# Kernel tuning notes

Measured on AMD Instinct MI355X. Metric: run time of the kernel, lower is better.

## Reference

```python
import jax, jax.numpy as jnp
import numpy as np

D_MODEL = 1024
D_STATE = 16
D_CONV = 4
D_INNER = 2 * D_MODEL          # expand * d_model
DT_RANK = (D_MODEL + 15) // 16 # ceil(d_model/16) = 64
BATCH, SEQLEN = 2, 1024


def setup_inputs() -> dict:
    key = jax.random.key(0)
    ks = jax.random.split(key, 8)
    s = lambda k, shape, scale=0.02: (jax.random.normal(k, shape, jnp.float32) * scale)
    return {
        "hidden_states": jax.random.normal(ks[0], (BATCH, SEQLEN, D_MODEL), jnp.float32),
        "in_proj_w": s(ks[1], (2 * D_INNER, D_MODEL)),
        "conv_w": s(ks[2], (D_INNER, 1, D_CONV), 0.3),   # depthwise conv kernel (O, I/groups=1, K)
        "conv_b": jnp.zeros((D_INNER,), jnp.float32),
        "x_proj_w": s(ks[3], (DT_RANK + 2 * D_STATE, D_INNER)),
        "dt_proj_w": s(ks[4], (D_INNER, DT_RANK), 0.1),
        # inverse-softplus of small dt values, like the torch init
        "dt_proj_b": jax.random.uniform(ks[5], (D_INNER,), jnp.float32, minval=-5.0, maxval=-2.0),
        "A_log": jnp.log(jnp.broadcast_to(jnp.arange(1, D_STATE + 1, dtype=jnp.float32), (D_INNER, D_STATE))),
        "D": jnp.ones((D_INNER,), jnp.float32),
        "out_proj_w": s(ks[6], (D_MODEL, D_INNER)),
    }


def _forward(hidden_states, in_proj_w, conv_w, conv_b, x_proj_w,
             dt_proj_w, dt_proj_b, A_log, D, out_proj_w):
    B, L, _ = hidden_states.shape
    # in_proj -> split into x, z
    xz = hidden_states @ in_proj_w.T                      # [B, L, 2*d_inner]
    x, z = jnp.split(xz, 2, axis=-1)
    # causal depthwise conv1d (pad left d_conv-1, then take first L) + SiLU
    xc = jnp.transpose(x, (0, 2, 1))                      # [B, d_inner, L]
    xc = jax.lax.conv_general_dilated(
        xc, conv_w, window_strides=(1,), padding=[(D_CONV - 1, 0)],
        feature_group_count=D_INNER,
        dimension_numbers=("NCH", "OIH", "NCH")) + conv_b[None, :, None]
    xc = jax.nn.silu(xc)
    u = jnp.transpose(xc, (0, 2, 1)).astype(jnp.float32)  # [B, L, d_inner]
    # x_proj -> dt_low, B, C
    x_dbl = u @ x_proj_w.T                                # [B, L, dt_rank + 2*d_state]
    dt_low, Bp, Cp = jnp.split(x_dbl, [DT_RANK, DT_RANK + D_STATE], axis=-1)
    dt = dt_low @ dt_proj_w.T + dt_proj_b                 # [B, L, d_inner]
    # NOTE: original adds dt_proj.bias AGAIN as delta_bias inside the scan, then softplus
    delta = jax.nn.softplus(dt + dt_proj_b)
    A = -jnp.exp(A_log.astype(jnp.float32))               # [d_inner, d_state]
    # discretization
    dA = jnp.exp(jnp.einsum("bld,dn->lbdn", delta, A))    # [L, B, d, n]
    dBu = jnp.einsum("bld,bln,bld->lbdn", delta, Bp.astype(jnp.float32), u)
    C_t = jnp.transpose(Cp.astype(jnp.float32), (1, 0, 2))  # [L, B, n]

    def step(state, inp):
        a, b, c = inp
        state = a * state + b                             # [B, d, n]
        y = jnp.einsum("bdn,bn->bd", state, c)
        return state, y

    x0 = jnp.zeros((B, D_INNER, D_STATE), jnp.float32)
    _, ys = jax.lax.scan(step, x0, (dA, dBu, C_t))        # ys: [L, B, d]
    y = jnp.transpose(ys, (1, 0, 2))                      # [B, L, d]
    y = y + u * D.astype(jnp.float32)                     # skip connection
    y = y * jax.nn.silu(z.astype(jnp.float32))            # gating
    y = y.astype(hidden_states.dtype)
    return y @ out_proj_w.T                               # [B, L, d_model]


def reference(hidden_states, in_proj_w, conv_w, conv_b, x_proj_w,
              dt_proj_w, dt_proj_b, A_log, D, out_proj_w):
    return _forward(hidden_states, in_proj_w, conv_w, conv_b, x_proj_w,
                    dt_proj_w, dt_proj_b, A_log, D, out_proj_w)
```

## Files before the change

kernel.cpp:

```cpp
#include <hip/hip_runtime.h>
#include <hip/hip_bf16.h>
#include <math.h>

#define BATCH   2
#define SEQLEN  1024
#define DMODEL  1024
#define DINNER  2048
#define DSTATE  16
#define DTRANK  64
#define XPAD    128
#define MROWS   (BATCH*SEQLEN)
#define NSEG    8
#define SEGLEN  (SEQLEN/NSEG)
#define XP_SPLIT  8
#define OUT_SPLIT 2

typedef float    f32x4  __attribute__((ext_vector_type(4)));
typedef _Float16 f16x8  __attribute__((ext_vector_type(8)));
typedef _Float16 f16x4  __attribute__((ext_vector_type(4)));

template<int EPI>
__global__ __launch_bounds__(256) void pgemm64(
    const _Float16* __restrict__ A, int lda,
    const _Float16* __restrict__ W, int ldw,
    float* __restrict__ C, int ldc, int K,
    const float* __restrict__ bias, _Float16* __restrict__ C16, size_t zstride)
{
  constexpr int APS = 520;
  constexpr int BPS = 1032;
  __shared__ _Float16 As[2][8 * APS];
  __shared__ _Float16 Bs[2][8 * BPS];

  const int t  = threadIdx.x;
  const int m0 = blockIdx.y * 64, n0 = blockIdx.x * 128;
  const int kchunk = K / gridDim.z;
  const int kbeg = blockIdx.z * kchunk;
  const int nIter = kchunk / 64;

  const int kb = t & 7;
  const int r0 = t >> 3;
  const _Float16* gA = A + (size_t)(m0 + r0) * lda + kbeg + kb * 8;
  const _Float16* gB = W + (size_t)(n0 + r0) * ldw + kbeg + kb * 8;
  const size_t a32 = (size_t)32 * lda;
  const size_t b32 = (size_t)32 * ldw;
  const int aoff = kb * APS + r0 * 8;
  const int boff = kb * BPS + r0 * 8;

  {
    f16x8 a0 = *(const f16x8*)(gA);
    f16x8 a1 = *(const f16x8*)(gA + a32);
    f16x8 b0 = *(const f16x8*)(gB);
    f16x8 b1 = *(const f16x8*)(gB + b32);
    f16x8 b2 = *(const f16x8*)(gB + 2 * b32);
    f16x8 b3 = *(const f16x8*)(gB + 3 * b32);
    gA += 64; gB += 64;
    *(f16x8*)&As[0][aoff]       = a0;
    *(f16x8*)&As[0][aoff + 256] = a1;
    *(f16x8*)&Bs[0][boff]       = b0;
    *(f16x8*)&Bs[0][boff + 256] = b1;
    *(f16x8*)&Bs[0][boff + 512] = b2;
    *(f16x8*)&Bs[0][boff + 768] = b3;
  }

  const int lane = t & 63, wvi = t >> 6;
  const int wn = wvi * 32;
  const int lm = lane & 15, lk = lane >> 4;

  f32x4 acc[4][2] = {};

  for (int it = 0; it < nIter; ++it) {
    __syncthreads();
    const bool more = (it + 1 < nIter);
    f16x8 a0, a1, b0, b1, b2, b3;
    if (more) {
      a0 = *(const f16x8*)(gA);
      a1 = *(const f16x8*)(gA + a32);
      b0 = *(const f16x8*)(gB);
      b1 = *(const f16x8*)(gB + b32);
      b2 = *(const f16x8*)(gB + 2 * b32);
      b3 = *(const f16x8*)(gB + 3 * b32);
      gA += 64; gB += 64;
    }
    const int cb = it & 1;
#pragma unroll
    for (int s = 0; s < 2; ++s) {
      f16x8 av[4], bv[2];
#pragma unroll
      for (int i = 0; i < 4; ++i)
        av[i] = *(const f16x8*)&As[cb][(s * 4 + lk) * APS + (i * 16 + lm) * 8];
#pragma unroll
      for (int j = 0; j < 2; ++j)
        bv[j] = *(const f16x8*)&Bs[cb][(s * 4 + lk) * BPS + (wn + j * 16 + lm) * 8];
#pragma unroll
      for (int i = 0; i < 4; ++i)
#pragma unroll
        for (int j = 0; j < 2; ++j)
          acc[i][j] = __builtin_amdgcn_mfma_f32_16x16x32_f16(av[i], bv[j], acc[i][j], 0, 0, 0);
    }
    if (more) {
      const int nb = (it + 1) & 1;
      *(f16x8*)&As[nb][aoff]       = a0;
      *(f16x8*)&As[nb][aoff + 256] = a1;
      *(f16x8*)&Bs[nb][boff]       = b0;
      *(f16x8*)&Bs[nb][boff + 256] = b1;
      *(f16x8*)&Bs[nb][boff + 512] = b2;
      *(f16x8*)&Bs[nb][boff + 768] = b3;
    }
  }

  float* Cz = C + (size_t)blockIdx.z * zstride;
#pragma unroll
  for (int i = 0; i < 4; ++i) {
    const int mrow = m0 + i * 16 + lk * 4;
#pragma unroll
    for (int j = 0; j < 2; ++j) {
      const int col = n0 + wn + j * 16 + lm;
#pragma unroll
      for (int r = 0; r < 4; ++r) {
        float v = acc[i][j][r];
        size_t off = (size_t)(mrow + r) * ldc + col;
        if constexpr (EPI == 0) {
          Cz[off] = v;
        } else {
          float x = v + 2.f * bias[col];
          float sp = (x > 80.f) ? x : __logf(1.f + __expf(x));
          C16[off] = (_Float16)sp;
        }
      }
    }
  }
}

template<int EPI>
__global__ __launch_bounds__(256) void pgemm128(
    const _Float16* __restrict__ A, int lda,
    const _Float16* __restrict__ W, int ldw,
    float* __restrict__ C, int ldc, int K,
    _Float16* __restrict__ C16, size_t zstride)
{
  constexpr int PS = 1032;
  __shared__ _Float16 As[2][8 * PS];
  __shared__ _Float16 Bs[2][8 * PS];

  const int t  = threadIdx.x;
  const int m0 = blockIdx.y * 128, n0 = blockIdx.x * 128;
  const int kchunk = K / gridDim.z;
  const int kbeg = blockIdx.z * kchunk;
  const int nIter = kchunk / 64;

  const int kb = t & 7;
  const int r0 = t >> 3;
  const _Float16* gA = A + (size_t)(m0 + r0) * lda + kbeg + kb * 8;
  const _Float16* gB = W + (size_t)(n0 + r0) * ldw + kbeg + kb * 8;
  const size_t a32 = (size_t)32 * lda;
  const size_t b32 = (size_t)32 * ldw;
  const int soff = kb * PS + r0 * 8;

  {
    f16x8 ar[4], br[4];
#pragma unroll
    for (int j = 0; j < 4; ++j) {
      ar[j] = *(const f16x8*)(gA + j * a32);
      br[j] = *(const f16x8*)(gB + j * b32);
    }
    gA += 64; gB += 64;
#pragma unroll
    for (int j = 0; j < 4; ++j) {
      *(f16x8*)&As[0][soff + j * 256] = ar[j];
      *(f16x8*)&Bs[0][soff + j * 256] = br[j];
    }
  }

  const int lane = t & 63, wvi = t >> 6;
  const int wm = (wvi >> 1) * 64, wn = (wvi & 1) * 64;
  const int lm = lane & 15, lk = lane >> 4;

  f32x4 acc[4][4] = {};

  for (int it = 0; it < nIter; ++it) {
    __syncthreads();
    const bool more = (it + 1 < nIter);
    f16x8 ar[4], br[4];
    if (more) {
#pragma unroll
      for (int j = 0; j < 4; ++j) {
        ar[j] = *(const f16x8*)(gA + j * a32);
        br[j] = *(const f16x8*)(gB + j * b32);
      }
      gA += 64; gB += 64;
    }
    const int cb = it & 1;
#pragma unroll
    for (int s = 0; s < 2; ++s) {
      f16x8 av[4], bv[4];
#pragma unroll
      for (int i = 0; i < 4; ++i)
        av[i] = *(const f16x8*)&As[cb][(s * 4 + lk) * PS + (wm + i * 16 + lm) * 8];
#pragma unroll
      for (int j = 0; j < 4; ++j)
        bv[j] = *(const f16x8*)&Bs[cb][(s * 4 + lk) * PS + (wn + j * 16 + lm) * 8];
#pragma unroll
      for (int i = 0; i < 4; ++i)
#pragma unroll
        for (int j = 0; j < 4; ++j)
          acc[i][j] = __builtin_amdgcn_mfma_f32_16x16x32_f16(av[i], bv[j], acc[i][j], 0, 0, 0);
    }
    if (more) {
      const int nb = (it + 1) & 1;
#pragma unroll
      for (int j = 0; j < 4; ++j) {
        *(f16x8*)&As[nb][soff + j * 256] = ar[j];
        *(f16x8*)&Bs[nb][soff + j * 256] = br[j];
      }
    }
  }

  float* Cz = C + (size_t)blockIdx.z * zstride;
#pragma unroll
  for (int i = 0; i < 4; ++i) {
    const int mrow = m0 + wm + i * 16 + lk * 4;
#pragma unroll
    for (int j = 0; j < 4; ++j) {
      const int col = n0 + wn + j * 16 + lm;
#pragma unroll
      for (int r = 0; r < 4; ++r) {
        float v = acc[i][j][r];
        size_t off = (size_t)(mrow + r) * ldc + col;
        if constexpr (EPI == 0) {
          Cz[off] = v;
        } else {
          C16[off] = (_Float16)v;
        }
      }
    }
  }
}

#define R0 (MROWS * DMODEL / 4)
#define R1 (2 * DINNER * DMODEL / 4)
#define R2 (DMODEL * DINNER / 4)
#define R3 (DINNER * DTRANK / 4)
#define R4 (XPAD * DINNER / 4)
#define F2H_TOTAL (R0 + R1 + R2 + R3 + R4)

__global__ __launch_bounds__(256) void f2h_all(
    const float* __restrict__ hid, const float* __restrict__ w_in,
    const float* __restrict__ w_out, const float* __restrict__ w_dt,
    const float* __restrict__ w_xp,
    _Float16* __restrict__ hid16, _Float16* __restrict__ w_in16,
    _Float16* __restrict__ w_out16, _Float16* __restrict__ w_dt16,
    _Float16* __restrict__ w_xp16)
{
  int i = blockIdx.x * 256 + threadIdx.x;
  const float* src; _Float16* dst; int off;
  if (i < R0)                     { src = hid;   dst = hid16;   off = i; }
  else if (i < R0+R1)             { src = w_in;  dst = w_in16;  off = i - R0; }
  else if (i < R0+R1+R2)          { src = w_out; dst = w_out16; off = i - (R0+R1); }
  else if (i < R0+R1+R2+R3)       { src = w_dt;  dst = w_dt16;  off = i - (R0+R1+R2); }
  else if (i < F2H_TOTAL) {
    off = i - (R0+R1+R2+R3);
    int r = (off * 4) >> 11;
    f16x4 h = {0, 0, 0, 0};
    if (r < 96) {
      float4 v = ((const float4*)w_xp)[off];
      h = (f16x4){(_Float16)v.x, (_Float16)v.y, (_Float16)v.z, (_Float16)v.w};
    }
    ((f16x4*)w_xp16)[off] = h;
    return;
  } else return;
  float4 v = ((const float4*)src)[off];
  ((f16x4*)dst)[off] = (f16x4){(_Float16)v.x, (_Float16)v.y, (_Float16)v.z, (_Float16)v.w};
}

__global__ __launch_bounds__(256) void reduce_xdbl(
    const float* __restrict__ part,
    float* __restrict__ xdbl32, _Float16* __restrict__ xdbl16)
{
  int i = blockIdx.x * 256 + threadIdx.x;
  f32x4 s = ((const f32x4*)part)[i];
#pragma unroll
  for (int z = 1; z < XP_SPLIT; ++z)
    s += ((const f32x4*)part)[(size_t)z * (MROWS * XPAD / 4) + i];
  ((f32x4*)xdbl32)[i] = s;
  int col4 = (i & 31) * 4;
  if (col4 < DTRANK) {
    int row = i >> 5;
    *(f16x4*)&xdbl16[(size_t)row * DTRANK + col4] =
        (f16x4){(_Float16)s.x, (_Float16)s.y, (_Float16)s.z, (_Float16)s.w};
  }
}

__global__ __launch_bounds__(256) void reduce_out(
    const float* __restrict__ part, float* __restrict__ out)
{
  int i = blockIdx.x * 256 + threadIdx.x;
  f32x4 s = ((const f32x4*)part)[i];
#pragma unroll
  for (int z = 1; z < OUT_SPLIT; ++z)
    s += ((const f32x4*)part)[(size_t)z * (MROWS * DMODEL / 4) + i];
  ((f32x4*)out)[i] = s;
}

__global__ __launch_bounds__(256) void conv_silu(
    const _Float16* __restrict__ xz16,
    const float* __restrict__ conv_w,
    const float* __restrict__ conv_b,
    _Float16* __restrict__ u16)
{
  const int idx = blockIdx.x * 256 + threadIdx.x;
  const int d   = idx & (DINNER - 1);
  const int row = idx >> 11;
  const int l   = row & (SEQLEN - 1);
  float s = conv_b[d];
#pragma unroll
  for (int k = 0; k < 4; ++k) {
    int lt = l + k - 3;
    if (lt >= 0)
      s = fmaf((float)xz16[(size_t)(row + k - 3) * (2 * DINNER) + d],
               conv_w[d * 4 + k], s);
  }
  float v = s / (1.f + __expf(-s));
  u16[idx] = (_Float16)v;
}

__device__ __forceinline__ float row_sum16(float x) {
  int v = __builtin_bit_cast(int, x);
  x += __builtin_bit_cast(float, __builtin_amdgcn_update_dpp(0, v, 0x128, 0xF, 0xF, true));
  v = __builtin_bit_cast(int, x);
  x += __builtin_bit_cast(float, __builtin_amdgcn_update_dpp(0, v, 0x124, 0xF, 0xF, true));
  v = __builtin_bit_cast(int, x);
  x += __builtin_bit_cast(float, __builtin_amdgcn_update_dpp(0, v, 0x4E, 0xF, 0xF, true));
  v = __builtin_bit_cast(int, x);
  x += __builtin_bit_cast(float, __builtin_amdgcn_update_dpp(0, v, 0xB1, 0xF, 0xF, true));
  return x;
}

__global__ __launch_bounds__(256) void scan_part1(
    const _Float16* __restrict__ delta16,
    const _Float16* __restrict__ u16,
    const float* __restrict__ x_dbl,
    const float* __restrict__ A_log,
    float* __restrict__ pbuf, float* __restrict__ ebuf)
{
  const int t = threadIdx.x;
  const int c = t >> 4, n = t & 15;
  const int bb = blockIdx.x;
  const int seg = bb >> 8;
  const int r = bb & 255;
  const int b = r >> 7;
  const int d_base = (r & 127) * 16;

  const float A_dn = -__expf(A_log[(d_base + c) * DSTATE + n]);
  float s = 0.f, p = 1.f;

  __shared__ __align__(16) float dl[16 * 68];
  __shared__ __align__(16) float ul[16 * 68];
  __shared__ __align__(16) float Bl[16 * 68];

  const int i_st = t >> 2;
  const int cc = (t & 3) * 4;

  for (int l0 = seg * SEGLEN; l0 < seg * SEGLEN + SEGLEN; l0 += 64) {
    const int row = b * SEQLEN + l0 + i_st;
    {
      f16x4  dh = *(const f16x4*)&delta16[(size_t)row * DINNER + d_base + cc];
      f16x4  uh = *(const f16x4*)&u16[(size_t)row * DINNER + d_base + cc];
      float4 Bv = *(const float4*)&x_dbl[(size_t)row * XPAD + DTRANK + cc];
      dl[(cc+0)*68 + i_st] = (float)dh[0]; dl[(cc+1)*68 + i_st] = (float)dh[1];
      dl[(cc+2)*68 + i_st] = (float)dh[2]; dl[(cc+3)*68 + i_st] = (float)dh[3];
      ul[(cc+0)*68 + i_st] = (float)uh[0]; ul[(cc+1)*68 + i_st] = (float)uh[1];
      ul[(cc+2)*68 + i_st] = (float)uh[2]; ul[(cc+3)*68 + i_st] = (float)uh[3];
      Bl[(cc+0)*68 + i_st] = Bv.x; Bl[(cc+1)*68 + i_st] = Bv.y;
      Bl[(cc+2)*68 + i_st] = Bv.z; Bl[(cc+3)*68 + i_st] = Bv.w;
    }
    __syncthreads();
#pragma unroll
    for (int i0 = 0; i0 < 64; i0 += 4) {
      f32x4 dv4 = *(const f32x4*)&dl[c * 68 + i0];
      f32x4 uv4 = *(const f32x4*)&ul[c * 68 + i0];
      f32x4 Bv4 = *(const f32x4*)&Bl[n * 68 + i0];
#pragma unroll
      for (int rr = 0; rr < 4; ++rr) {
        float dA = __expf(dv4[rr] * A_dn);
        s = fmaf(dA, s, dv4[rr] * Bv4[rr] * uv4[rr]);
        p *= dA;
      }
    }
    __syncthreads();
  }
  const int peIdx = (r * NSEG + seg) * 256 + t;
  pbuf[peIdx] = p;
  ebuf[peIdx] = s;
}

__global__ __launch_bounds__(256) void scan_part2(
    const _Float16* __restrict__ delta16,
    const _Float16* __restrict__ u16,
    const _Float16* __restrict__ xz16,
    const float* __restrict__ x_dbl,
    const float* __restrict__ A_log,
    const float* __restrict__ Dp,
    const float* __restrict__ pbuf,
    const float* __restrict__ ebuf,
    _Float16* __restrict__ y16)
{
  const int t = threadIdx.x;
  const int c = t >> 4, n = t & 15;
  const int bb = blockIdx.x;
  const int seg = bb >> 8;
  const int r = bb & 255;
  const int b = r >> 7;
  const int d_base = (r & 127) * 16;

  const float A_dn = -__expf(A_log[(d_base + c) * DSTATE + n]);

  float s = 0.f;
  {
    const int base = r * NSEG * 256 + t;
    for (int k = 0; k < seg; ++k)
      s = fmaf(pbuf[base + k * 256], s, ebuf[base + k * 256]);
  }

  __shared__ __align__(16) float dl[16 * 68];
  __shared__ __align__(16) float ul[16 * 68];
  __shared__ __align__(16) float Bl[16 * 68];
  __shared__ __align__(16) float Cl[16 * 68];
  __shared__ __align__(16) float yl[16 * 68];
  __shared__ __align__(16) float z_s[64 * 16];
  __shared__ float Dp_s[16];

  if (t < 16) Dp_s[t] = Dp[d_base + t];

  const int i_st = t >> 2;
  const int cc = (t & 3) * 4;

  for (int l0 = seg * SEGLEN; l0 < seg * SEGLEN + SEGLEN; l0 += 64) {
    const int row = b * SEQLEN + l0 + i_st;
    {
      f16x4  dh = *(const f16x4*)&delta16[(size_t)row * DINNER + d_base + cc];
      f16x4  uh = *(const f16x4*)&u16[(size_t)row * DINNER + d_base + cc];
      float4 Bv = *(const float4*)&x_dbl[(size_t)row * XPAD + DTRANK + cc];
      float4 Cv = *(const float4*)&x_dbl[(size_t)row * XPAD + DTRANK + DSTATE + cc];
      f16x4  zh = *(const f16x4*)&xz16[(size_t)row * (2 * DINNER) + DINNER + d_base + cc];
      dl[(cc+0)*68 + i_st] = (float)dh[0]; dl[(cc+1)*68 + i_st] = (float)dh[1];
      dl[(cc+2)*68 + i_st] = (float)dh[2]; dl[(cc+3)*68 + i_st] = (float)dh[3];
      ul[(cc+0)*68 + i_st] = (float)uh[0]; ul[(cc+1)*68 + i_st] = (float)uh[1];
      ul[(cc+2)*68 + i_st] = (float)uh[2]; ul[(cc+3)*68 + i_st] = (float)uh[3];
      Bl[(cc+0)*68 + i_st] = Bv.x; Bl[(cc+1)*68 + i_st] = Bv.y;
      Bl[(cc+2)*68 + i_st] = Bv.z; Bl[(cc+3)*68 + i_st] = Bv.w;
      Cl[(cc+0)*68 + i_st] = Cv.x; Cl[(cc+1)*68 + i_st] = Cv.y;
      Cl[(cc+2)*68 + i_st] = Cv.z; Cl[(cc+3)*68 + i_st] = Cv.w;
      float4 zv = make_float4((float)zh[0], (float)zh[1], (float)zh[2], (float)zh[3]);
      *(float4*)&z_s[t * 4] = zv;
    }
    __syncthreads();

#pragma unroll
    for (int i0 = 0; i0 < 64; i0 += 4) {
      f32x4 dv4 = *(const f32x4*)&dl[c * 68 + i0];
      f32x4 uv4 = *(const f32x4*)&ul[c * 68 + i0];
      f32x4 Bv4 = *(const f32x4*)&Bl[n * 68 + i0];
      f32x4 Cv4 = *(const f32x4*)&Cl[n * 68 + i0];
      f32x4 py;
#pragma unroll
      for (int rr = 0; rr < 4; ++rr) {
        float dA = __expf(dv4[rr] * A_dn);
        s = fmaf(dA, s, dv4[rr] * Bv4[rr] * uv4[rr]);
        py[rr] = row_sum16(s * Cv4[rr]);
      }
      if (n == 0) *(f32x4*)&yl[c * 68 + i0] = py;
    }
    __syncthreads();

#pragma unroll
    for (int k = 0; k < 4; ++k) {
      int o = t + 256 * k;
      int i = o >> 4, c2 = o & 15;
      float ssum = yl[c2 * 68 + i];
      float uv = ul[c2 * 68 + i];
      float zv = z_s[o];
      float yv = fmaf(uv, Dp_s[c2], ssum);
      yv *= zv / (1.f + __expf(-zv));
      y16[(size_t)(b * SEQLEN + l0 + i) * DINNER + d_base + c2] = (_Float16)yv;
    }
    __syncthreads();
  }
}

extern "C" void kernel_launch(void* const* d_in, const int* in_sizes, int n_in,
                              void* d_out, int out_size, void* d_ws, size_t ws_size,
                              hipStream_t stream)
{
  const float* hidden     = (const float*)d_in[0];
  const float* in_proj_w  = (const float*)d_in[1];
  const float* conv_w     = (const float*)d_in[2];
  const float* conv_b     = (const float*)d_in[3];
  const float* x_proj_w   = (const float*)d_in[4];
  const float* dt_proj_w  = (const float*)d_in[5];
  const float* dt_proj_b  = (const float*)d_in[6];
  const float* A_log      = (const float*)d_in[7];
  const float* Dp         = (const float*)d_in[8];
  const float* out_proj_w = (const float*)d_in[9];
  float* out = (float*)d_out;

  char* p = (char*)d_ws;
  _Float16* xz16    = (_Float16*)p;  p += (size_t)MROWS * 2 * DINNER * 2;
  _Float16* u16     = (_Float16*)p;  p += (size_t)MROWS * DINNER * 2;
  float*    xdbl32  = (float*)p;     p += (size_t)MROWS * XPAD * 4;
  _Float16* delta16 = (_Float16*)p;  p += (size_t)MROWS * DINNER * 2;
  _Float16* h16     = (_Float16*)p;  p += (size_t)MROWS * DMODEL * 2;
  _Float16* win16   = (_Float16*)p;  p += (size_t)2 * DINNER * DMODEL * 2;
  _Float16* wout16  = (_Float16*)p;  p += (size_t)DMODEL * DINNER * 2;
  _Float16* wdt16   = (_Float16*)p;  p += (size_t)DINNER * DTRANK * 2;
  _Float16* wxp16   = (_Float16*)p;  p += (size_t)XPAD * DINNER * 2;
  _Float16* xdbl16  = (_Float16*)p;  p += (size_t)MROWS * DTRANK * 2;
  _Float16* y16     = (_Float16*)p;  p += (size_t)MROWS * DINNER * 2;
  float*    pbuf    = (float*)p;     p += (size_t)256 * NSEG * 256 * 4;
  float*    ebuf    = (float*)p;     p += (size_t)256 * NSEG * 256 * 4;
  float*    xp_part  = (float*)delta16;
  float*    out_part = (float*)xz16;

  f2h_all<<<(F2H_TOTAL + 255) / 256, 256, 0, stream>>>(
      hidden, in_proj_w, out_proj_w, dt_proj_w, x_proj_w,
      h16, win16, wout16, wdt16, wxp16);

  pgemm128<4><<<dim3(4096 / 128, MROWS / 128, 1), 256, 0, stream>>>(
      h16, DMODEL, win16, DMODEL, nullptr, 4096, DMODEL, xz16, 0);

  conv_silu<<<(MROWS * DINNER) / 256, 256, 0, stream>>>(xz16, conv_w, conv_b, u16);

  pgemm64<0><<<dim3(1, MROWS / 64, XP_SPLIT), 256, 0, stream>>>(
      u16, DINNER, wxp16, DINNER, xp_part, XPAD, DINNER, nullptr, nullptr,
      (size_t)MROWS * XPAD);

  reduce_xdbl<<<(MROWS * XPAD / 4) / 256, 256, 0, stream>>>(xp_part, xdbl32, xdbl16);

  pgemm64<2><<<dim3(DINNER / 128, MROWS / 64, 1), 256, 0, stream>>>(
      xdbl16, DTRANK, wdt16, DTRANK, nullptr, DINNER, DTRANK, dt_proj_b, delta16, 0);

  scan_part1<<<256 * NSEG, 256, 0, stream>>>(delta16, u16, xdbl32, A_log, pbuf, ebuf);
  scan_part2<<<256 * NSEG, 256, 0, stream>>>(delta16, u16, xz16, xdbl32, A_log, Dp,
                                             pbuf, ebuf, y16);

  pgemm128<0><<<dim3(DMODEL / 128, MROWS / 128, OUT_SPLIT), 256, 0, stream>>>(
      y16, DINNER, wout16, DINNER, out_part, DMODEL, DINNER, nullptr,
      (size_t)MROWS * DMODEL);

  reduce_out<<<(MROWS * DMODEL / 4) / 256, 256, 0, stream>>>(out_part, out);
}
```

Before: 228.7 us.

## Fuse dt_proj matmul and softplus into scan_part1, drop separate GEMM

Computes delta = softplus(x_dbl[:, :64] @ dt_proj_w^T + 2*bias) inside scan_part1 with fp32 FMAs from shared memory, and writes delta16 back for scan_part2. This removes the dt_proj GEMM launch, the fp16 xdbl copy and the dt weight conversion, and keeps delta in fp32 for the part1 recurrence. In exchange each scan block now runs a 64x16x64 scalar matmul per chunk and uses more shared memory (about 17KB more), which may lower occupancy and makes part1 heavier. The softplus cutoff also moves from 80 to 20.

```diff
diff --git a/kernel.cpp b/kernel.cpp
--- a/kernel.cpp
+++ b/kernel.cpp
@@ -122,9 +122,7 @@
         if constexpr (EPI == 0) {
           Cz[off] = v;
         } else {
-          float x = v + 2.f * bias[col];
-          float sp = (x > 80.f) ? x : __logf(1.f + __expf(x));
-          C16[off] = (_Float16)sp;
+          C16[off] = (_Float16)v;
         }
       }
     }
@@ -239,26 +237,22 @@
 #define R0 (MROWS * DMODEL / 4)
 #define R1 (2 * DINNER * DMODEL / 4)
 #define R2 (DMODEL * DINNER / 4)
-#define R3 (DINNER * DTRANK / 4)
 #define R4 (XPAD * DINNER / 4)
-#define F2H_TOTAL (R0 + R1 + R2 + R3 + R4)
+#define F2H_TOTAL (R0 + R1 + R2 + R4)
 
 __global__ __launch_bounds__(256) void f2h_all(
     const float* __restrict__ hid, const float* __restrict__ w_in,
-    const float* __restrict__ w_out, const float* __restrict__ w_dt,
-    const float* __restrict__ w_xp,
+    const float* __restrict__ w_out, const float* __restrict__ w_xp,
     _Float16* __restrict__ hid16, _Float16* __restrict__ w_in16,
-    _Float16* __restrict__ w_out16, _Float16* __restrict__ w_dt16,
-    _Float16* __restrict__ w_xp16)
+    _Float16* __restrict__ w_out16, _Float16* __restrict__ w_xp16)
 {
   int i = blockIdx.x * 256 + threadIdx.x;
   const float* src; _Float16* dst; int off;
   if (i < R0)                     { src = hid;   dst = hid16;   off = i; }
   else if (i < R0+R1)             { src = w_in;  dst = w_in16;  off = i - R0; }
   else if (i < R0+R1+R2)          { src = w_out; dst = w_out16; off = i - (R0+R1); }
-  else if (i < R0+R1+R2+R3)       { src = w_dt;  dst = w_dt16;  off = i - (R0+R1+R2); }
   else if (i < F2H_TOTAL) {
-    off = i - (R0+R1+R2+R3);
+    off = i - (R0+R1+R2);
     int r = (off * 4) >> 11;
     f16x4 h = {0, 0, 0, 0};
     if (r < 96) {
@@ -274,7 +268,7 @@
 
 __global__ __launch_bounds__(256) void reduce_xdbl(
     const float* __restrict__ part,
-    float* __restrict__ xdbl32, _Float16* __restrict__ xdbl16)
+    float* __restrict__ xdbl32)
 {
   int i = blockIdx.x * 256 + threadIdx.x;
   f32x4 s = ((const f32x4*)part)[i];
@@ -282,12 +276,6 @@
   for (int z = 1; z < XP_SPLIT; ++z)
     s += ((const f32x4*)part)[(size_t)z * (MROWS * XPAD / 4) + i];
   ((f32x4*)xdbl32)[i] = s;
-  int col4 = (i & 31) * 4;
-  if (col4 < DTRANK) {
-    int row = i >> 5;
-    *(f16x4*)&xdbl16[(size_t)row * DTRANK + col4] =
-        (f16x4){(_Float16)s.x, (_Float16)s.y, (_Float16)s.z, (_Float16)s.w};
-  }
 }
 
 __global__ __launch_bounds__(256) void reduce_out(
@@ -336,11 +324,13 @@
 }
 
 __global__ __launch_bounds__(256) void scan_part1(
-    const _Float16* __restrict__ delta16,
     const _Float16* __restrict__ u16,
     const float* __restrict__ x_dbl,
     const float* __restrict__ A_log,
-    float* __restrict__ pbuf, float* __restrict__ ebuf)
+    const float* __restrict__ dt_w,
+    const float* __restrict__ dt_b,
+    float* __restrict__ pbuf, float* __restrict__ ebuf,
+    _Float16* __restrict__ delta16)
 {
   const int t = threadIdx.x;
   const int c = t >> 4, n = t & 15;
@@ -356,24 +346,67 @@
   __shared__ __align__(16) float dl[16 * 68];
   __shared__ __align__(16) float ul[16 * 68];
   __shared__ __align__(16) float Bl[16 * 68];
+  __shared__ __align__(16) float xd[64 * 68];
+  __shared__ __align__(16) float wt[16 * 68];
+  __shared__ float db2[16];
+
+  {
+    const int c0 = t >> 4, k0 = (t & 15) * 4;
+    *(float4*)&wt[c0 * 68 + k0] =
+        *(const float4*)&dt_w[(size_t)(d_base + c0) * DTRANK + k0];
+    if (t < 16) db2[t] = 2.f * dt_b[d_base + t];
+  }
 
   const int i_st = t >> 2;
   const int cc = (t & 3) * 4;
+  const int xr = t >> 2;
+  const int xc = (t & 3) * 16;
 
   for (int l0 = seg * SEGLEN; l0 < seg * SEGLEN + SEGLEN; l0 += 64) {
-    const int row = b * SEQLEN + l0 + i_st;
+    const int rowbase = b * SEQLEN + l0;
+    const int row = rowbase + i_st;
     {
-      f16x4  dh = *(const f16x4*)&delta16[(size_t)row * DINNER + d_base + cc];
       f16x4  uh = *(const f16x4*)&u16[(size_t)row * DINNER + d_base + cc];
       float4 Bv = *(const float4*)&x_dbl[(size_t)row * XPAD + DTRANK + cc];
-      dl[(cc+0)*68 + i_st] = (float)dh[0]; dl[(cc+1)*68 + i_st] = (float)dh[1];
-      dl[(cc+2)*68 + i_st] = (float)dh[2]; dl[(cc+3)*68 + i_st] = (float)dh[3];
       ul[(cc+0)*68 + i_st] = (float)uh[0]; ul[(cc+1)*68 + i_st] = (float)uh[1];
       ul[(cc+2)*68 + i_st] = (float)uh[2]; ul[(cc+3)*68 + i_st] = (float)uh[3];
       Bl[(cc+0)*68 + i_st] = Bv.x; Bl[(cc+1)*68 + i_st] = Bv.y;
       Bl[(cc+2)*68 + i_st] = Bv.z; Bl[(cc+3)*68 + i_st] = Bv.w;
-    }
-    __syncthreads();
+      const float* xrow = &x_dbl[(size_t)(rowbase + xr) * XPAD + xc];
+      float4 x0 = ((const float4*)xrow)[0];
+      float4 x1 = ((const float4*)xrow)[1];
+      float4 x2 = ((const float4*)xrow)[2];
+      float4 x3 = ((const float4*)xrow)[3];
+      *(float4*)&xd[xr * 68 + xc +  0] = x0;
+      *(float4*)&xd[xr * 68 + xc +  4] = x1;
+      *(float4*)&xd[xr * 68 + xc +  8] = x2;
+      *(float4*)&xd[xr * 68 + xc + 12] = x3;
+    }
+    __syncthreads();
+
+    {
+      const float b2 = db2[c];
+      float a0 = b2, a1 = b2, a2 = b2, a3 = b2;
+      const float* wrow = &wt[c * 68];
+#pragma unroll
+      for (int k = 0; k < 64; ++k) {
+        float w = wrow[k];
+        a0 = fmaf(xd[(n     ) * 68 + k], w, a0);
+        a1 = fmaf(xd[(n + 16) * 68 + k], w, a1);
+        a2 = fmaf(xd[(n + 32) * 68 + k], w, a2);
+        a3 = fmaf(xd[(n + 48) * 68 + k], w, a3);
+      }
+      a0 = (a0 > 20.f) ? a0 : __logf(1.f + __expf(a0));
+      a1 = (a1 > 20.f) ? a1 : __logf(1.f + __expf(a1));
+      a2 = (a2 > 20.f) ? a2 : __logf(1.f + __expf(a2));
+      a3 = (a3 > 20.f) ? a3 : __logf(1.f + __expf(a3));
+      dl[c * 68 + n     ] = a0;
+      dl[c * 68 + n + 16] = a1;
+      dl[c * 68 + n + 32] = a2;
+      dl[c * 68 + n + 48] = a3;
+    }
+    __syncthreads();
+
 #pragma unroll
     for (int i0 = 0; i0 < 64; i0 += 4) {
       f32x4 dv4 = *(const f32x4*)&dl[c * 68 + i0];
@@ -385,6 +418,13 @@
         s = fmaf(dA, s, dv4[rr] * Bv4[rr] * uv4[rr]);
         p *= dA;
       }
+    }
+
+#pragma unroll
+    for (int kk = 0; kk < 4; ++kk) {
+      int o = t + 256 * kk;
+      int i = o >> 4, c2 = o & 15;
+      delta16[(size_t)(rowbase + i) * DINNER + d_base + c2] = (_Float16)dl[c2 * 68 + i];
     }
     __syncthreads();
   }
@@ -511,9 +551,7 @@
   _Float16* h16     = (_Float16*)p;  p += (size_t)MROWS * DMODEL * 2;
   _Float16* win16   = (_Float16*)p;  p += (size_t)2 * DINNER * DMODEL * 2;
   _Float16* wout16  = (_Float16*)p;  p += (size_t)DMODEL * DINNER * 2;
-  _Float16* wdt16   = (_Float16*)p;  p += (size_t)DINNER * DTRANK * 2;
   _Float16* wxp16   = (_Float16*)p;  p += (size_t)XPAD * DINNER * 2;
-  _Float16* xdbl16  = (_Float16*)p;  p += (size_t)MROWS * DTRANK * 2;
   _Float16* y16     = (_Float16*)p;  p += (size_t)MROWS * DINNER * 2;
   float*    pbuf    = (float*)p;     p += (size_t)256 * NSEG * 256 * 4;
   float*    ebuf    = (float*)p;     p += (size_t)256 * NSEG * 256 * 4;
@@ -521,8 +559,8 @@
   float*    out_part = (float*)xz16;
 
   f2h_all<<<(F2H_TOTAL + 255) / 256, 256, 0, stream>>>(
-      hidden, in_proj_w, out_proj_w, dt_proj_w, x_proj_w,
-      h16, win16, wout16, wdt16, wxp16);
+      hidden, in_proj_w, out_proj_w, x_proj_w,
+      h16, win16, wout16, wxp16);
 
   pgemm128<4><<<dim3(4096 / 128, MROWS / 128, 1), 256, 0, stream>>>(
       h16, DMODEL, win16, DMODEL, nullptr, 4096, DMODEL, xz16, 0);
@@ -533,12 +571,10 @@
       u16, DINNER, wxp16, DINNER, xp_part, XPAD, DINNER, nullptr, nullptr,
       (size_t)MROWS * XPAD);
 
-  reduce_xdbl<<<(MROWS * XPAD / 4) / 256, 256, 0, stream>>>(xp_part, xdbl32, xdbl16);
-
-  pgemm64<2><<<dim3(DINNER / 128, MROWS / 64, 1), 256, 0, stream>>>(
-      xdbl16, DTRANK, wdt16, DTRANK, nullptr, DINNER, DTRANK, dt_proj_b, delta16, 0);
-
-  scan_part1<<<256 * NSEG, 256, 0, stream>>>(delta16, u16, xdbl32, A_log, pbuf, ebuf);
+  reduce_xdbl<<<(MROWS * XPAD / 4) / 256, 256, 0, stream>>>(xp_part, xdbl32);
+
+  scan_part1<<<256 * NSEG, 256, 0, stream>>>(u16, xdbl32, A_log, dt_proj_w,
+                                             dt_proj_b, pbuf, ebuf, delta16);
   scan_part2<<<256 * NSEG, 256, 0, stream>>>(delta16, u16, xz16, xdbl32, A_log, Dp,
                                              pbuf, ebuf, y16);
 
```

After: 243.1 us. 6.3% more time.

## Store delta transposed and load it directly into scan registers

Applied to the files above, without the earlier changes.

The dt_proj GEMM epilogue now writes softplus(delta) in a transposed [d_inner, rows] layout using 4-wide half stores. The scan kernels then read each channel's delta run as contiguous f16x8 vectors straight into registers, which removes the delta shared-memory staging and its LDS reads. Each of the 16 state lanes of a channel loads the same delta values, so global traffic for delta is duplicated, though it should mostly be served from cache. The softplus overflow threshold also changes from 80 to 20.

```diff
diff --git a/kernel.cpp b/kernel.cpp
--- a/kernel.cpp
+++ b/kernel.cpp
@@ -115,17 +115,20 @@
 #pragma unroll
     for (int j = 0; j < 2; ++j) {
       const int col = n0 + wn + j * 16 + lm;
-#pragma unroll
-      for (int r = 0; r < 4; ++r) {
-        float v = acc[i][j][r];
-        size_t off = (size_t)(mrow + r) * ldc + col;
-        if constexpr (EPI == 0) {
-          Cz[off] = v;
-        } else {
-          float x = v + 2.f * bias[col];
-          float sp = (x > 80.f) ? x : __logf(1.f + __expf(x));
-          C16[off] = (_Float16)sp;
+      if constexpr (EPI == 2) {
+        const float b2 = 2.f * bias[col];
+        f16x4 h;
+#pragma unroll
+        for (int r = 0; r < 4; ++r) {
+          float x = acc[i][j][r] + b2;
+          float sp = (x > 20.f) ? x : __logf(1.f + __expf(x));
+          h[r] = (_Float16)sp;
         }
+        *(f16x4*)&C16[(size_t)col * MROWS + mrow] = h;
+      } else {
+#pragma unroll
+        for (int r = 0; r < 4; ++r)
+          Cz[(size_t)(mrow + r) * ldc + col] = acc[i][j][r];
       }
     }
   }
@@ -336,7 +339,7 @@
 }
 
 __global__ __launch_bounds__(256) void scan_part1(
-    const _Float16* __restrict__ delta16,
+    const _Float16* __restrict__ deltaT,
     const _Float16* __restrict__ u16,
     const float* __restrict__ x_dbl,
     const float* __restrict__ A_log,
@@ -353,21 +356,21 @@
   const float A_dn = -__expf(A_log[(d_base + c) * DSTATE + n]);
   float s = 0.f, p = 1.f;
 
-  __shared__ __align__(16) float dl[16 * 68];
   __shared__ __align__(16) float ul[16 * 68];
   __shared__ __align__(16) float Bl[16 * 68];
 
   const int i_st = t >> 2;
   const int cc = (t & 3) * 4;
+  const _Float16* dT = deltaT + (size_t)(d_base + c) * MROWS + b * SEQLEN;
 
   for (int l0 = seg * SEGLEN; l0 < seg * SEGLEN + SEGLEN; l0 += 64) {
     const int row = b * SEQLEN + l0 + i_st;
+    f16x8 dreg[8];
+#pragma unroll
+    for (int q = 0; q < 8; ++q) dreg[q] = *(const f16x8*)(dT + l0 + q * 8);
     {
-      f16x4  dh = *(const f16x4*)&delta16[(size_t)row * DINNER + d_base + cc];
       f16x4  uh = *(const f16x4*)&u16[(size_t)row * DINNER + d_base + cc];
       float4 Bv = *(const float4*)&x_dbl[(size_t)row * XPAD + DTRANK + cc];
-      dl[(cc+0)*68 + i_st] = (float)dh[0]; dl[(cc+1)*68 + i_st] = (float)dh[1];
-      dl[(cc+2)*68 + i_st] = (float)dh[2]; dl[(cc+3)*68 + i_st] = (float)dh[3];
       ul[(cc+0)*68 + i_st] = (float)uh[0]; ul[(cc+1)*68 + i_st] = (float)uh[1];
       ul[(cc+2)*68 + i_st] = (float)uh[2]; ul[(cc+3)*68 + i_st] = (float)uh[3];
       Bl[(cc+0)*68 + i_st] = Bv.x; Bl[(cc+1)*68 + i_st] = Bv.y;
@@ -376,13 +379,15 @@
     __syncthreads();
 #pragma unroll
     for (int i0 = 0; i0 < 64; i0 += 4) {
-      f32x4 dv4 = *(const f32x4*)&dl[c * 68 + i0];
       f32x4 uv4 = *(const f32x4*)&ul[c * 68 + i0];
       f32x4 Bv4 = *(const f32x4*)&Bl[n * 68 + i0];
+      f16x8 dr = dreg[i0 >> 3];
+      const int e0 = i0 & 7;
 #pragma unroll
       for (int rr = 0; rr < 4; ++rr) {
-        float dA = __expf(dv4[rr] * A_dn);
-        s = fmaf(dA, s, dv4[rr] * Bv4[rr] * uv4[rr]);
+        float dv = (float)dr[e0 + rr];
+        float dA = __expf(dv * A_dn);
+        s = fmaf(dA, s, dv * Bv4[rr] * uv4[rr]);
         p *= dA;
       }
     }
@@ -394,7 +399,7 @@
 }
 
 __global__ __launch_bounds__(256) void scan_part2(
-    const _Float16* __restrict__ delta16,
+    const _Float16* __restrict__ deltaT,
     const _Float16* __restrict__ u16,
     const _Float16* __restrict__ xz16,
     const float* __restrict__ x_dbl,
@@ -421,7 +426,6 @@
       s = fmaf(pbuf[base + k * 256], s, ebuf[base + k * 256]);
   }
 
-  __shared__ __align__(16) float dl[16 * 68];
   __shared__ __align__(16) float ul[16 * 68];
   __shared__ __align__(16) float Bl[16 * 68];
   __shared__ __align__(16) float Cl[16 * 68];
@@ -433,17 +437,18 @@
 
   const int i_st = t >> 2;
   const int cc = (t & 3) * 4;
+  const _Float16* dT = deltaT + (size_t)(d_base + c) * MROWS + b * SEQLEN;
 
   for (int l0 = seg * SEGLEN; l0 < seg * SEGLEN + SEGLEN; l0 += 64) {
     const int row = b * SEQLEN + l0 + i_st;
+    f16x8 dreg[8];
+#pragma unroll
+    for (int q = 0; q < 8; ++q) dreg[q] = *(const f16x8*)(dT + l0 + q * 8);
     {
-      f16x4  dh = *(const f16x4*)&delta16[(size_t)row * DINNER + d_base + cc];
       f16x4  uh = *(const f16x4*)&u16[(size_t)row * DINNER + d_base + cc];
       float4 Bv = *(const float4*)&x_dbl[(size_t)row * XPAD + DTRANK + cc];
       float4 Cv = *(const float4*)&x_dbl[(size_t)row * XPAD + DTRANK + DSTATE + cc];
       f16x4  zh = *(const f16x4*)&xz16[(size_t)row * (2 * DINNER) + DINNER + d_base + cc];
-      dl[(cc+0)*68 + i_st] = (float)dh[0]; dl[(cc+1)*68 + i_st] = (float)dh[1];
-      dl[(cc+2)*68 + i_st] = (float)dh[2]; dl[(cc+3)*68 + i_st] = (float)dh[3];
       ul[(cc+0)*68 + i_st] = (float)uh[0]; ul[(cc+1)*68 + i_st] = (float)uh[1];
       ul[(cc+2)*68 + i_st] = (float)uh[2]; ul[(cc+3)*68 + i_st] = (float)uh[3];
       Bl[(cc+0)*68 + i_st] = Bv.x; Bl[(cc+1)*68 + i_st] = Bv.y;
@@ -457,15 +462,17 @@
 
 #pragma unroll
     for (int i0 = 0; i0 < 64; i0 += 4) {
-      f32x4 dv4 = *(const f32x4*)&dl[c * 68 + i0];
       f32x4 uv4 = *(const f32x4*)&ul[c * 68 + i0];
       f32x4 Bv4 = *(const f32x4*)&Bl[n * 68 + i0];
       f32x4 Cv4 = *(const f32x4*)&Cl[n * 68 + i0];
+      f16x8 dr = dreg[i0 >> 3];
+      const int e0 = i0 & 7;
       f32x4 py;
 #pragma unroll
       for (int rr = 0; rr < 4; ++rr) {
-        float dA = __expf(dv4[rr] * A_dn);
-        s = fmaf(dA, s, dv4[rr] * Bv4[rr] * uv4[rr]);
+        float dv = (float)dr[e0 + rr];
+        float dA = __expf(dv * A_dn);
+        s = fmaf(dA, s, dv * Bv4[rr] * uv4[rr]);
         py[rr] = row_sum16(s * Cv4[rr]);
       }
       if (n == 0) *(f32x4*)&yl[c * 68 + i0] = py;
@@ -507,7 +514,7 @@
   _Float16* xz16    = (_Float16*)p;  p += (size_t)MROWS * 2 * DINNER * 2;
   _Float16* u16     = (_Float16*)p;  p += (size_t)MROWS * DINNER * 2;
   float*    xdbl32  = (float*)p;     p += (size_t)MROWS * XPAD * 4;
-  _Float16* delta16 = (_Float16*)p;  p += (size_t)MROWS * DINNER * 2;
+  _Float16* deltaT  = (_Float16*)p;  p += (size_t)MROWS * DINNER * 2;
   _Float16* h16     = (_Float16*)p;  p += (size_t)MROWS * DMODEL * 2;
   _Float16* win16   = (_Float16*)p;  p += (size_t)2 * DINNER * DMODEL * 2;
   _Float16* wout16  = (_Float16*)p;  p += (size_t)DMODEL * DINNER * 2;
@@ -517,7 +524,7 @@
   _Float16* y16     = (_Float16*)p;  p += (size_t)MROWS * DINNER * 2;
   float*    pbuf    = (float*)p;     p += (size_t)256 * NSEG * 256 * 4;
   float*    ebuf    = (float*)p;     p += (size_t)256 * NSEG * 256 * 4;
-  float*    xp_part  = (float*)delta16;
+  float*    xp_part  = (float*)deltaT;
   float*    out_part = (float*)xz16;
 
   f2h_all<<<(F2H_TOTAL + 255) / 256, 256, 0, stream>>>(
@@ -536,10 +543,10 @@
   reduce_xdbl<<<(MROWS * XPAD / 4) / 256, 256, 0, stream>>>(xp_part, xdbl32, xdbl16);
 
   pgemm64<2><<<dim3(DINNER / 128, MROWS / 64, 1), 256, 0, stream>>>(
-      xdbl16, DTRANK, wdt16, DTRANK, nullptr, DINNER, DTRANK, dt_proj_b, delta16, 0);
-
-  scan_part1<<<256 * NSEG, 256, 0, stream>>>(delta16, u16, xdbl32, A_log, pbuf, ebuf);
-  scan_part2<<<256 * NSEG, 256, 0, stream>>>(delta16, u16, xz16, xdbl32, A_log, Dp,
+      xdbl16, DTRANK, wdt16, DTRANK, nullptr, DINNER, DTRANK, dt_proj_b, deltaT, 0);
+
+  scan_part1<<<256 * NSEG, 256, 0, stream>>>(deltaT, u16, xdbl32, A_log, pbuf, ebuf);
+  scan_part2<<<256 * NSEG, 256, 0, stream>>>(deltaT, u16, xz16, xdbl32, A_log, Dp,
                                              pbuf, ebuf, y16);
 
   pgemm128<0><<<dim3(DMODEL / 128, MROWS / 128, OUT_SPLIT), 256, 0, stream>>>(
```

Result: no change. 229.7 us (+0.4%).

## Restructure selective scan to thread-per-channel with 64 segments and separate carry pass

Applied to the files above, without the earlier changes.

Replaces the thread-per-(channel,state) scan, which used DPP row reductions over 16 lanes, with a layout where each thread owns one channel and keeps all 16 states in registers. The sequence is split into 64 segments instead of 8. A new scan_mid kernel computes each segment's carry-in state serially across segments, and the per-segment decay is derived as exp(sum(delta)*A) instead of a running product. This removes the cross-lane reductions and the shared-memory transposes and exposes more parallelism. The cost is larger intermediate buffers (pbuf, ebuf, cbuf), an extra launch, and serial global-memory traffic in the mid pass. It also lowers the softplus cutoff from 80 to 20, a minor numerical tweak.

```diff
diff --git a/kernel.cpp b/kernel.cpp
--- a/kernel.cpp
+++ b/kernel.cpp
@@ -10,8 +10,8 @@
 #define DTRANK  64
 #define XPAD    128
 #define MROWS   (BATCH*SEQLEN)
-#define NSEG    8
-#define SEGLEN  (SEQLEN/NSEG)
+#define NSEG2   64
+#define SEGL2   (SEQLEN/NSEG2)
 #define XP_SPLIT  8
 #define OUT_SPLIT 2
 
@@ -123,7 +123,7 @@
           Cz[off] = v;
         } else {
           float x = v + 2.f * bias[col];
-          float sp = (x > 80.f) ? x : __logf(1.f + __expf(x));
+          float sp = (x > 20.f) ? x : __logf(1.f + __expf(x));
           C16[off] = (_Float16)sp;
         }
       }
@@ -323,19 +323,7 @@
   u16[idx] = (_Float16)v;
 }
 
-__device__ __forceinline__ float row_sum16(float x) {
-  int v = __builtin_bit_cast(int, x);
-  x += __builtin_bit_cast(float, __builtin_amdgcn_update_dpp(0, v, 0x128, 0xF, 0xF, true));
-  v = __builtin_bit_cast(int, x);
-  x += __builtin_bit_cast(float, __builtin_amdgcn_update_dpp(0, v, 0x124, 0xF, 0xF, true));
-  v = __builtin_bit_cast(int, x);
-  x += __builtin_bit_cast(float, __builtin_amdgcn_update_dpp(0, v, 0x4E, 0xF, 0xF, true));
-  v = __builtin_bit_cast(int, x);
-  x += __builtin_bit_cast(float, __builtin_amdgcn_update_dpp(0, v, 0xB1, 0xF, 0xF, true));
-  return x;
-}
-
-__global__ __launch_bounds__(256) void scan_part1(
+__global__ __launch_bounds__(256) void scan_pe(
     const _Float16* __restrict__ delta16,
     const _Float16* __restrict__ u16,
     const float* __restrict__ x_dbl,
@@ -343,147 +331,131 @@
     float* __restrict__ pbuf, float* __restrict__ ebuf)
 {
   const int t = threadIdx.x;
-  const int c = t >> 4, n = t & 15;
-  const int bb = blockIdx.x;
-  const int seg = bb >> 8;
-  const int r = bb & 255;
-  const int b = r >> 7;
-  const int d_base = (r & 127) * 16;
-
-  const float A_dn = -__expf(A_log[(d_base + c) * DSTATE + n]);
-  float s = 0.f, p = 1.f;
-
-  __shared__ __align__(16) float dl[16 * 68];
-  __shared__ __align__(16) float ul[16 * 68];
-  __shared__ __align__(16) float Bl[16 * 68];
-
-  const int i_st = t >> 2;
-  const int cc = (t & 3) * 4;
-
-  for (int l0 = seg * SEGLEN; l0 < seg * SEGLEN + SEGLEN; l0 += 64) {
-    const int row = b * SEQLEN + l0 + i_st;
-    {
-      f16x4  dh = *(const f16x4*)&delta16[(size_t)row * DINNER + d_base + cc];
-      f16x4  uh = *(const f16x4*)&u16[(size_t)row * DINNER + d_base + cc];
-      float4 Bv = *(const float4*)&x_dbl[(size_t)row * XPAD + DTRANK + cc];
-      dl[(cc+0)*68 + i_st] = (float)dh[0]; dl[(cc+1)*68 + i_st] = (float)dh[1];
-      dl[(cc+2)*68 + i_st] = (float)dh[2]; dl[(cc+3)*68 + i_st] = (float)dh[3];
-      ul[(cc+0)*68 + i_st] = (float)uh[0]; ul[(cc+1)*68 + i_st] = (float)uh[1];
-      ul[(cc+2)*68 + i_st] = (float)uh[2]; ul[(cc+3)*68 + i_st] = (float)uh[3];
-      Bl[(cc+0)*68 + i_st] = Bv.x; Bl[(cc+1)*68 + i_st] = Bv.y;
-      Bl[(cc+2)*68 + i_st] = Bv.z; Bl[(cc+3)*68 + i_st] = Bv.w;
-    }
-    __syncthreads();
-#pragma unroll
-    for (int i0 = 0; i0 < 64; i0 += 4) {
-      f32x4 dv4 = *(const f32x4*)&dl[c * 68 + i0];
-      f32x4 uv4 = *(const f32x4*)&ul[c * 68 + i0];
-      f32x4 Bv4 = *(const f32x4*)&Bl[n * 68 + i0];
-#pragma unroll
-      for (int rr = 0; rr < 4; ++rr) {
-        float dA = __expf(dv4[rr] * A_dn);
-        s = fmaf(dA, s, dv4[rr] * Bv4[rr] * uv4[rr]);
-        p *= dA;
-      }
-    }
-    __syncthreads();
-  }
-  const int peIdx = (r * NSEG + seg) * 256 + t;
-  pbuf[peIdx] = p;
-  ebuf[peIdx] = s;
-}
-
-__global__ __launch_bounds__(256) void scan_part2(
+  const int d = blockIdx.x * 256 + t;
+  const int b   = blockIdx.y >> 6;
+  const int seg = blockIdx.y & 63;
+  const int row0 = b * SEQLEN + seg * SEGL2;
+
+  float A_dn[DSTATE];
+#pragma unroll
+  for (int q = 0; q < 4; ++q) {
+    f32x4 a4 = *(const f32x4*)&A_log[(size_t)d * DSTATE + q * 4];
+#pragma unroll
+    for (int e = 0; e < 4; ++e) A_dn[q * 4 + e] = -__expf(a4[e]);
+  }
+
+  __shared__ __align__(16) float Bl[SEGL2 * DSTATE];
+  if (t < 64) {
+    int i = t >> 2, n4 = (t & 3) * 4;
+    *(f32x4*)&Bl[i * DSTATE + n4] =
+        *(const f32x4*)&x_dbl[(size_t)(row0 + i) * XPAD + DTRANK + n4];
+  }
+  __syncthreads();
+
+  float E[DSTATE];
+#pragma unroll
+  for (int n = 0; n < DSTATE; ++n) E[n] = 0.f;
+  float S = 0.f;
+
+  for (int i = 0; i < SEGL2; ++i) {
+    const size_t ro = (size_t)(row0 + i) * DINNER + d;
+    float dv = (float)delta16[ro];
+    float uv = (float)u16[ro];
+    float du = dv * uv;
+    S += dv;
+#pragma unroll
+    for (int n = 0; n < DSTATE; ++n) {
+      float dA = __expf(dv * A_dn[n]);
+      E[n] = fmaf(dA, E[n], du * Bl[i * DSTATE + n]);
+    }
+  }
+
+  const size_t base = ((size_t)(b * NSEG2 + seg) * DSTATE) * DINNER + d;
+#pragma unroll
+  for (int n = 0; n < DSTATE; ++n) {
+    pbuf[base + (size_t)n * DINNER] = __expf(S * A_dn[n]);
+    ebuf[base + (size_t)n * DINNER] = E[n];
+  }
+}
+
+__global__ __launch_bounds__(256) void scan_mid(
+    const float* __restrict__ pbuf, const float* __restrict__ ebuf,
+    float* __restrict__ cbuf)
+{
+  const int idx = blockIdx.x * 256 + threadIdx.x;
+  const int d = idx & (DINNER - 1);
+  const int n = (idx >> 11) & 15;
+  const int b = idx >> 15;
+  float s = 0.f;
+  for (int seg = 0; seg < NSEG2; ++seg) {
+    const size_t off = ((size_t)(b * NSEG2 + seg) * DSTATE + n) * DINNER + d;
+    cbuf[off] = s;
+    s = fmaf(pbuf[off], s, ebuf[off]);
+  }
+}
+
+__global__ __launch_bounds__(256) void scan_y(
     const _Float16* __restrict__ delta16,
     const _Float16* __restrict__ u16,
     const _Float16* __restrict__ xz16,
     const float* __restrict__ x_dbl,
     const float* __restrict__ A_log,
     const float* __restrict__ Dp,
-    const float* __restrict__ pbuf,
-    const float* __restrict__ ebuf,
+    const float* __restrict__ cbuf,
     _Float16* __restrict__ y16)
 {
   const int t = threadIdx.x;
-  const int c = t >> 4, n = t & 15;
-  const int bb = blockIdx.x;
-  const int seg = bb >> 8;
-  const int r = bb & 255;
-  const int b = r >> 7;
-  const int d_base = (r & 127) * 16;
-
-  const float A_dn = -__expf(A_log[(d_base + c) * DSTATE + n]);
-
-  float s = 0.f;
+  const int d = blockIdx.x * 256 + t;
+  const int b   = blockIdx.y >> 6;
+  const int seg = blockIdx.y & 63;
+  const int row0 = b * SEQLEN + seg * SEGL2;
+
+  float A_dn[DSTATE];
+#pragma unroll
+  for (int q = 0; q < 4; ++q) {
+    f32x4 a4 = *(const f32x4*)&A_log[(size_t)d * DSTATE + q * 4];
+#pragma unroll
+    for (int e = 0; e < 4; ++e) A_dn[q * 4 + e] = -__expf(a4[e]);
+  }
+  const float Dv = Dp[d];
+
+  __shared__ __align__(16) float Bl[SEGL2 * DSTATE];
+  __shared__ __align__(16) float Cl[SEGL2 * DSTATE];
+  if (t < 64) {
+    int i = t >> 2, n4 = (t & 3) * 4;
+    *(f32x4*)&Bl[i * DSTATE + n4] =
+        *(const f32x4*)&x_dbl[(size_t)(row0 + i) * XPAD + DTRANK + n4];
+  } else if (t < 128) {
+    int u = t - 64;
+    int i = u >> 2, n4 = (u & 3) * 4;
+    *(f32x4*)&Cl[i * DSTATE + n4] =
+        *(const f32x4*)&x_dbl[(size_t)(row0 + i) * XPAD + DTRANK + DSTATE + n4];
+  }
+  __syncthreads();
+
+  float s[DSTATE];
   {
-    const int base = r * NSEG * 256 + t;
-    for (int k = 0; k < seg; ++k)
-      s = fmaf(pbuf[base + k * 256], s, ebuf[base + k * 256]);
-  }
-
-  __shared__ __align__(16) float dl[16 * 68];
-  __shared__ __align__(16) float ul[16 * 68];
-  __shared__ __align__(16) float Bl[16 * 68];
-  __shared__ __align__(16) float Cl[16 * 68];
-  __shared__ __align__(16) float yl[16 * 68];
-  __shared__ __align__(16) float z_s[64 * 16];
-  __shared__ float Dp_s[16];
-
-  if (t < 16) Dp_s[t] = Dp[d_base + t];
-
-  const int i_st = t >> 2;
-  const int cc = (t & 3) * 4;
-
-  for (int l0 = seg * SEGLEN; l0 < seg * SEGLEN + SEGLEN; l0 += 64) {
-    const int row = b * SEQLEN + l0 + i_st;
-    {
-      f16x4  dh = *(const f16x4*)&delta16[(size_t)row * DINNER + d_base + cc];
-      f16x4  uh = *(const f16x4*)&u16[(size_t)row * DINNER + d_base + cc];
-      float4 Bv = *(const float4*)&x_dbl[(size_t)row * XPAD + DTRANK + cc];
-      float4 Cv = *(const float4*)&x_dbl[(size_t)row * XPAD + DTRANK + DSTATE + cc];
-      f16x4  zh = *(const f16x4*)&xz16[(size_t)row * (2 * DINNER) + DINNER + d_base + cc];
-      dl[(cc+0)*68 + i_st] = (float)dh[0]; dl[(cc+1)*68 + i_st] = (float)dh[1];
-      dl[(cc+2)*68 + i_st] = (float)dh[2]; dl[(cc+3)*68 + i_st] = (float)dh[3];
-      ul[(cc+0)*68 + i_st] = (float)uh[0]; ul[(cc+1)*68 + i_st] = (float)uh[1];
-      ul[(cc+2)*68 + i_st] = (float)uh[2]; ul[(cc+3)*68 + i_st] = (float)uh[3];
-      Bl[(cc+0)*68 + i_st] = Bv.x; Bl[(cc+1)*68 + i_st] = Bv.y;
-      Bl[(cc+2)*68 + i_st] = Bv.z; Bl[(cc+3)*68 + i_st] = Bv.w;
-      Cl[(cc+0)*68 + i_st] = Cv.x; Cl[(cc+1)*68 + i_st] = Cv.y;
-      Cl[(cc+2)*68 + i_st] = Cv.z; Cl[(cc+3)*68 + i_st] = Cv.w;
-      float4 zv = make_float4((float)zh[0], (float)zh[1], (float)zh[2], (float)zh[3]);
-      *(float4*)&z_s[t * 4] = zv;
-    }
-    __syncthreads();
-
-#pragma unroll
-    for (int i0 = 0; i0 < 64; i0 += 4) {
-      f32x4 dv4 = *(const f32x4*)&dl[c * 68 + i0];
-      f32x4 uv4 = *(const f32x4*)&ul[c * 68 + i0];
-      f32x4 Bv4 = *(const f32x4*)&Bl[n * 68 + i0];
-      f32x4 Cv4 = *(const f32x4*)&Cl[n * 68 + i0];
-      f32x4 py;
-#pragma unroll
-      for (int rr = 0; rr < 4; ++rr) {
-        float dA = __expf(dv4[rr] * A_dn);
-        s = fmaf(dA, s, dv4[rr] * Bv4[rr] * uv4[rr]);
-        py[rr] = row_sum16(s * Cv4[rr]);
-      }
-      if (n == 0) *(f32x4*)&yl[c * 68 + i0] = py;
-    }
-    __syncthreads();
-
-#pragma unroll
-    for (int k = 0; k < 4; ++k) {
-      int o = t + 256 * k;
-      int i = o >> 4, c2 = o & 15;
-      float ssum = yl[c2 * 68 + i];
-      float uv = ul[c2 * 68 + i];
-      float zv = z_s[o];
-      float yv = fmaf(uv, Dp_s[c2], ssum);
-      yv *= zv / (1.f + __expf(-zv));
-      y16[(size_t)(b * SEQLEN + l0 + i) * DINNER + d_base + c2] = (_Float16)yv;
-    }
-    __syncthreads();
+    const size_t base = ((size_t)(b * NSEG2 + seg) * DSTATE) * DINNER + d;
+#pragma unroll
+    for (int n = 0; n < DSTATE; ++n) s[n] = cbuf[base + (size_t)n * DINNER];
+  }
+
+  for (int i = 0; i < SEGL2; ++i) {
+    const size_t ro = (size_t)(row0 + i) * DINNER + d;
+    float dv = (float)delta16[ro];
+    float uv = (float)u16[ro];
+    float zv = (float)xz16[(size_t)(row0 + i) * (2 * DINNER) + DINNER + d];
+    float du = dv * uv;
+    float y = 0.f;
+#pragma unroll
+    for (int n = 0; n < DSTATE; ++n) {
+      float dA = __expf(dv * A_dn[n]);
+      s[n] = fmaf(dA, s[n], du * Bl[i * DSTATE + n]);
+      y = fmaf(s[n], Cl[i * DSTATE + n], y);
+    }
+    y = fmaf(uv, Dv, y);
+    y *= zv / (1.f + __expf(-zv));
+    y16[ro] = (_Float16)y;
   }
 }
 
@@ -515,8 +487,9 @@
   _Float16* wxp16   = (_Float16*)p;  p += (size_t)XPAD * DINNER * 2;
   _Float16* xdbl16  = (_Float16*)p;  p += (size_t)MROWS * DTRANK * 2;
   _Float16* y16     = (_Float16*)p;  p += (size_t)MROWS * DINNER * 2;
-  float*    pbuf    = (float*)p;     p += (size_t)256 * NSEG * 256 * 4;
-  float*    ebuf    = (float*)p;     p += (size_t)256 * NSEG * 256 * 4;
+  float*    pbuf    = (float*)p;     p += (size_t)BATCH * NSEG2 * DSTATE * DINNER * 4;
+  float*    ebuf    = (float*)p;     p += (size_t)BATCH * NSEG2 * DSTATE * DINNER * 4;
+  float*    cbuf    = (float*)p;     p += (size_t)BATCH * NSEG2 * DSTATE * DINNER * 4;
   float*    xp_part  = (float*)delta16;
   float*    out_part = (float*)xz16;
 
@@ -538,9 +511,11 @@
   pgemm64<2><<<dim3(DINNER / 128, MROWS / 64, 1), 256, 0, stream>>>(
       xdbl16, DTRANK, wdt16, DTRANK, nullptr, DINNER, DTRANK, dt_proj_b, delta16, 0);
 
-  scan_part1<<<256 * NSEG, 256, 0, stream>>>(delta16, u16, xdbl32, A_log, pbuf, ebuf);
-  scan_part2<<<256 * NSEG, 256, 0, stream>>>(delta16, u16, xz16, xdbl32, A_log, Dp,
-                                             pbuf, ebuf, y16);
+  scan_pe<<<dim3(DINNER / 256, BATCH * NSEG2), 256, 0, stream>>>(
+      delta16, u16, xdbl32, A_log, pbuf, ebuf);
+  scan_mid<<<(BATCH * DSTATE * DINNER) / 256, 256, 0, stream>>>(pbuf, ebuf, cbuf);
+  scan_y<<<dim3(DINNER / 256, BATCH * NSEG2), 256, 0, stream>>>(
+      delta16, u16, xz16, xdbl32, A_log, Dp, cbuf, y16);
 
   pgemm128<0><<<dim3(DMODEL / 128, MROWS / 128, OUT_SPLIT), 256, 0, stream>>>(
       y16, DINNER, wout16, DINNER, out_part, DMODEL, DINNER, nullptr,
```

Result: no change. 229.3 us (+0.2%).
